# Performance work log

Measured on AMD Instinct MI355X. Metric: run time of the kernel, lower is better.

## Reference

```python
import jax, jax.numpy as jnp
import numpy as np

G_NUM = 32768      # graphs
NPG = 32           # nodes per graph
EPG = 128          # edges per graph
H = 128            # hidden
N = G_NUM * NPG
E = G_NUM * EPG


def setup_inputs() -> dict:
    key = jax.random.key(0)
    ks = jax.random.split(key, 8)
    x = jax.random.normal(ks[0], (N, H), dtype=jnp.float32)
    W1 = jax.random.normal(ks[1], (H, H), dtype=jnp.float32) * (1.0 / np.sqrt(H))
    b1 = jnp.zeros((H,), jnp.float32)
    W2 = jax.random.normal(ks[2], (H, 2), dtype=jnp.float32) * (1.0 / np.sqrt(H))
    b2 = jnp.zeros((2,), jnp.float32)
    # standard gumbel noise for F.gumbel_softmax(tau=1)
    u = jax.random.uniform(ks[3], (N, 2), dtype=jnp.float32, minval=1e-6, maxval=1.0 - 1e-6)
    gumbel_noise = -jnp.log(-jnp.log(u))
    uniform_noise = jax.random.uniform(ks[4], (N, H), dtype=jnp.float32)  # torch.rand_like
    # intra-graph random edges: graph g owns nodes [g*NPG, (g+1)*NPG)
    offs = jnp.repeat(jnp.arange(G_NUM, dtype=jnp.int32) * NPG, EPG)
    src = offs + jax.random.randint(ks[5], (E,), 0, NPG, dtype=jnp.int32)
    dst = offs + jax.random.randint(ks[6], (E,), 0, NPG, dtype=jnp.int32)
    edge_index = jnp.stack([src, dst])
    batch = jnp.repeat(jnp.arange(G_NUM, dtype=jnp.int32), NPG)
    return {"x": x, "W1": W1, "b1": b1, "W2": W2, "b2": b2,
            "gumbel_noise": gumbel_noise, "uniform_noise": uniform_noise,
            "edge_index": edge_index, "batch": batch, "num_graphs": G_NUM}


def reference(x, W1, b1, W2, b2, gumbel_noise, uniform_noise, edge_index, batch, num_graphs):
    eps = 1e-7
    G = int(num_graphs)
    Hd = x.shape[1]
    seg = lambda v: jax.ops.segment_sum(v, batch, num_segments=G)
    counts = seg(jnp.ones((x.shape[0],), x.dtype))                  # [G]
    # detached per-graph std/mean (torch.std_mean, unbiased)
    sx = jax.lax.stop_gradient(x)
    mean = seg(sx) / counts[:, None]                                # [G,H]
    var = seg((sx - mean[batch]) ** 2) / (counts - 1.0)[:, None]
    std = jnp.sqrt(var)                                             # [G,H]
    # soft assignment + gumbel-softmax (tau=1, logits = softmax probs, as in source)
    abstract1 = jnp.tanh(x @ W1 + b1)
    assignment = jax.nn.softmax(abstract1 @ W2 + b2, axis=1)        # [N,2]
    gum = jax.nn.softmax(assignment + gumbel_noise, axis=-1)        # [N,2]
    lam_pos = gum[:, :1]
    lam_neg = gum[:, 1:2]
    mean_n = mean[batch]
    std_n = std[batch]
    noisy_mean = lam_pos * x + lam_neg * mean_n                     # [N,H]
    noisy_std = lam_neg * std_n                                     # [N,H]
    noisy = noisy_mean + uniform_noise * noisy_std
    graph_emb = seg(x)                                              # [G,H]
    noisy_emb = seg(noisy)                                          # [G,H]
    # KL: 0.5*noisy_std^2/(std+eps)^2 (per node) + sum_nodes(((noisy_mean-mean)/(std+eps))^2) (per graph, broadcast)
    term1 = 0.5 * noisy_std ** 2 / (std_n + eps) ** 2               # [N,H]
    term2 = seg(((noisy_mean - mean_n) / (std_n + eps)) ** 2)       # [G,H]
    kl_g = (jnp.sum(seg(term1), axis=1) + counts * jnp.sum(term2, axis=1)) / (counts * Hd)
    kl_loss = jnp.mean(kl_g)
    # pooled adjacency: assignment^T A assignment per graph, via edge list
    src, dst = edge_index[0], edge_index[1]
    e_g = batch[src]
    contrib = assignment[src][:, :, None] * assignment[dst][:, None, :]  # [E,2,2]
    new_adj = jax.ops.segment_sum(contrib, e_g, num_segments=G)          # [G,2,2]
    row_l1 = jnp.maximum(jnp.sum(jnp.abs(new_adj), axis=2, keepdims=True), 1e-12)
    norm_adj = new_adj / row_l1
    diag = jnp.diagonal(norm_adj, axis1=1, axis2=2)                 # [G,2]
    pos_penalty = jnp.mean(jnp.mean((diag - 1.0) ** 2, axis=1))
    preserve_g = seg((assignment[:, 0] > 0.5).astype(x.dtype)) / counts
    preserve_rate = jnp.mean(preserve_g)
    active = lam_pos[:, 0] > 0.5                                    # [N] node mask
    return graph_emb, noisy_emb, active, pos_penalty, kl_loss, preserve_rate
```

## Files before the change

### kernel.cpp

```cpp
#include <hip/hip_runtime.h>

#define HN   128
#define NPG  32
#define GP4  4
#define NT   512
#define SX   132
#define TILE (NPG * SX)

typedef float f4 __attribute__((ext_vector_type(4)));
typedef float f2 __attribute__((ext_vector_type(2)));

__global__ __launch_bounds__(NT, 2) void gib_main(
    const float* __restrict__ x,  const float* __restrict__ W1,
    const float* __restrict__ b1, const float* __restrict__ W2,
    const float* __restrict__ b2, const float* __restrict__ gn,
    const float* __restrict__ un, const int* __restrict__ ei,
    float* __restrict__ out, float* __restrict__ ws,
    int G, long E, int epg, int spb)
{
  const int t    = threadIdx.x;
  const int p    = t >> 7;
  const int lo   = t & 127;
  const int ng   = lo & 7;
  const int cg   = lo >> 3;
  const int wv   = t >> 6;
  const int lid  = t & 63;
  const int half = lo >> 6;
  const int fp   = lo & 63;

  __shared__ __align__(16) float W1s[HN * HN];
  __shared__ __align__(16) float xs[GP4 * TILE];
  __shared__ float zred[GP4][2][8][4][2];
  __shared__ float pA[GP4][2][HN], pB[GP4][2][HN];
  __shared__ float s_mean[GP4][HN], s_std[GP4][HN], s_iv[GP4][HN];
  __shared__ float s_a0[GP4][NPG], s_a1[GP4][NPG], s_lp[GP4][NPG], s_ln[GP4][NPG];
  __shared__ float t2p[GP4][2], sr2p[GP4], adjp[GP4][2][4], s_scal[GP4][3];

  const long GL = (long)G * HN;
  const int  g0 = blockIdx.x * (GP4 * spb);

  const f4 b1a = *(const f4*)(b1 + 8 * cg);
  const f4 b1b = *(const f4*)(b1 + 8 * cg + 4);
  float w2l[16];
  #pragma unroll
  for (int u = 0; u < 4; ++u) {
    f4 v = *(const f4*)(W2 + 16 * cg + 4 * u);
    w2l[4*u+0] = v[0]; w2l[4*u+1] = v[1]; w2l[4*u+2] = v[2]; w2l[4*u+3] = v[3];
  }
  const float b20 = b2[0], b21 = b2[1];

  #pragma unroll
  for (int r = 0; r < 8; ++r) {
    int s = r * NT + t;
    int k = s >> 5, gm = s & 31;
    int slot = ((gm & 1) << 4) | (gm >> 1);
    *(f4*)&W1s[k * HN + slot * 4] = *(const f4*)(W1 + s * 4);
  }
  #pragma unroll
  for (int r = 0; r < 8; ++r) {
    int s = r * NT + t;
    int pp = s >> 10, q = s & 1023, n = q >> 5, pc = q & 31;
    *(f4*)&xs[pp * TILE + n * SX + pc * 4] =
        *(const f4*)(x + ((long)(g0 + pp) * NPG + n) * HN + pc * 4);
  }
  __syncthreads();

  for (int si = 0; si < spb; ++si) {
    const int  gs = g0 + si * GP4;
    const int  g  = gs + p;
    const long nb = (long)g * NPG;
    const bool more = (si + 1 < spb);

    f4 xr[8];
    if (more) {
      #pragma unroll
      for (int r = 0; r < 8; ++r) {
        int s = r * NT + t;
        int pp = s >> 10, q = s & 1023, n = q >> 5, pc = q & 31;
        xr[r] = *(const f4*)(x + ((long)(gs + GP4 + pp) * NPG + n) * HN + pc * 4);
      }
    }
    f2 gnr = {0.f, 0.f};
    if (wv < GP4 && lid < NPG)
      gnr = *(const f2*)(gn + ((long)(gs + wv) * NPG + lid) * 2);

    {
      const float* xb = &xs[p * TILE + half * 16 * SX + 2 * fp];
      float s10 = 0.f, s11 = 0.f, s20 = 0.f, s21 = 0.f;
      #pragma unroll
      for (int it = 0; it < 16; ++it) {
        f2 v = *(const f2*)(xb + it * SX);
        s10 += v[0]; s11 += v[1];
        s20 = fmaf(v[0], v[0], s20);
        s21 = fmaf(v[1], v[1], s21);
      }
      f2 w0 = {s10, s11}, w1v = {s20, s21};
      *(f2*)&pA[p][half][2 * fp] = w0;
      *(f2*)&pB[p][half][2 * fp] = w1v;
    }

    f4 aa[4], ab[4];
    #pragma unroll
    for (int i = 0; i < 4; ++i) { aa[i] = b1a; ab[i] = b1b; }
    {
      const float* xb = &xs[p * TILE + ng * SX];
      const float* wb = &W1s[cg * 4];
      #pragma unroll 8
      for (int pc = 0; pc < 32; ++pc) {
        f4 xv0 = *(const f4*)(xb + pc * 4);
        f4 xv1 = *(const f4*)(xb + 8  * SX + pc * 4);
        f4 xv2 = *(const f4*)(xb + 16 * SX + pc * 4);
        f4 xv3 = *(const f4*)(xb + 24 * SX + pc * 4);
        #pragma unroll
        for (int j = 0; j < 4; ++j) {
          f4 wa  = *(const f4*)(wb + (4 * pc + j) * HN);
          f4 wbv = *(const f4*)(wb + (4 * pc + j) * HN + 64);
          aa[0] += wa * xv0[j]; ab[0] += wbv * xv0[j];
          aa[1] += wa * xv1[j]; ab[1] += wbv * xv1[j];
          aa[2] += wa * xv2[j]; ab[2] += wbv * xv2[j];
          aa[3] += wa * xv3[j]; ab[3] += wbv * xv3[j];
        }
      }
    }
    #pragma unroll
    for (int i = 0; i < 4; ++i) {
      float z0 = 0.f, z1 = 0.f;
      #pragma unroll
      for (int u = 0; u < 4; ++u) {
        float h = tanhf(aa[i][u]);
        z0 = fmaf(h, w2l[2 * u], z0);
        z1 = fmaf(h, w2l[2 * u + 1], z1);
      }
      #pragma unroll
      for (int u = 0; u < 4; ++u) {
        float h = tanhf(ab[i][u]);
        z0 = fmaf(h, w2l[8 + 2 * u], z0);
        z1 = fmaf(h, w2l[9 + 2 * u], z1);
      }
      #pragma unroll
      for (int m = 8; m <= 32; m <<= 1) {
        z0 += __shfl_xor(z0, m, 64);
        z1 += __shfl_xor(z1, m, 64);
      }
      if (lid < 8) { zred[p][half][ng][i][0] = z0; zred[p][half][ng][i][1] = z1; }
    }
    __syncthreads();

    if (wv < GP4) {
      const int gq = gs + wv;
      f2 sa0 = *(const f2*)&pA[wv][0][2 * lid];
      f2 sa1 = *(const f2*)&pA[wv][1][2 * lid];
      f2 sb0 = *(const f2*)&pB[wv][0][2 * lid];
      f2 sb1 = *(const f2*)&pB[wv][1][2 * lid];
      float s10 = sa0[0] + sa1[0], s11 = sa0[1] + sa1[1];
      float s20 = sb0[0] + sb1[0], s21 = sb0[1] + sb1[1];
      float mean0 = s10 * (1.f / NPG), mean1 = s11 * (1.f / NPG);
      float var0 = fmaxf((s20 - s10 * mean0) * (1.f / (NPG - 1)), 0.f);
      float var1 = fmaxf((s21 - s11 * mean1) * (1.f / (NPG - 1)), 0.f);
      float sd0 = sqrtf(var0), sd1 = sqrtf(var1);
      float inv0 = 1.f / (sd0 + 1e-7f), inv1 = 1.f / (sd1 + 1e-7f);
      f2 mv = {mean0, mean1}, sv = {sd0, sd1}, iv = {inv0 * inv0, inv1 * inv1};
      *(f2*)&s_mean[wv][2 * lid] = mv;
      *(f2*)&s_std [wv][2 * lid] = sv;
      *(f2*)&s_iv  [wv][2 * lid] = iv;
      f2 ge = {s10, s11};
      *(f2*)&out[(long)gq * HN + 2 * lid] = ge;
      float r0 = sd0 * inv0, r1 = sd1 * inv1;
      float r2 = r0 * r0 + r1 * r1;
      #pragma unroll
      for (int m = 1; m <= 32; m <<= 1) r2 += __shfl_xor(r2, m, 64);
      if (lid == 0) sr2p[wv] = r2;
      if (lid < NPG) {
        const int n = lid;
        float z0 = b20 + zred[wv][0][n & 7][n >> 3][0] + zred[wv][1][n & 7][n >> 3][0];
        float z1 = b21 + zred[wv][0][n & 7][n >> 3][1] + zred[wv][1][n & 7][n >> 3][1];
        float zm = fmaxf(z0, z1);
        float e0 = expf(z0 - zm), e1 = expf(z1 - zm);
        float a0 = e0 / (e0 + e1), a1 = 1.f - a0;
        float q0 = a0 + gnr[0], q1 = a1 + gnr[1];
        float qm = fmaxf(q0, q1);
        float E0 = expf(q0 - qm), E1 = expf(q1 - qm);
        float lp = E0 / (E0 + E1), ln = 1.f - lp;
        s_a0[wv][n] = a0; s_a1[wv][n] = a1; s_lp[wv][n] = lp; s_ln[wv][n] = ln;
        out[2 * GL + (long)gq * NPG + n] = (lp > 0.5f) ? 1.0f : 0.0f;
        float v1 = ln, v2 = ln * ln, v3 = (a0 > 0.5f) ? 1.f : 0.f;
        #pragma unroll
        for (int m = 1; m <= 16; m <<= 1) {
          v1 += __shfl_xor(v1, m, 64);
          v2 += __shfl_xor(v2, m, 64);
          v3 += __shfl_xor(v3, m, 64);
        }
        if (n == 0) { s_scal[wv][0] = v1; s_scal[wv][1] = v2; s_scal[wv][2] = v3; }
      }
    }
    __syncthreads();

    {
      f2 ur[16];
      #pragma unroll
      for (int it = 0; it < 16; ++it)
        ur[it] = *(const f2*)(un + (nb + half * 16 + it) * HN + 2 * fp);
      int es = 0, ed = 0;
      if (lo < epg) {
        es = ei[(long)g * epg + lo] - g * NPG;
        ed = ei[E + (long)g * epg + lo] - g * NPG;
      }
      const float* xb = &xs[p * TILE + half * 16 * SX + 2 * fp];
      f2 mu = *(const f2*)&s_mean[p][2 * fp];
      f2 iv = *(const f2*)&s_iv[p][2 * fp];
      float tv = 0.f, A0 = 0.f, A1 = 0.f, B0 = 0.f, B1 = 0.f;
      #pragma unroll
      for (int it = 0; it < 16; ++it) {
        const int n = half * 16 + it;
        f2 v = *(const f2*)(xb + it * SX);
        float lpn = s_lp[p][n], lnn = s_ln[p][n];
        float d0 = v[0] - mu[0], d1 = v[1] - mu[1];
        tv = fmaf(lpn * lpn, fmaf(d0 * d0, iv[0], d1 * d1 * iv[1]), tv);
        A0 = fmaf(lpn, v[0], A0); A1 = fmaf(lpn, v[1], A1);
        B0 = fmaf(lnn, ur[it][0], B0); B1 = fmaf(lnn, ur[it][1], B1);
      }
      #pragma unroll
      for (int m = 1; m <= 32; m <<= 1) tv += __shfl_xor(tv, m, 64);
      if (lid == 0) t2p[p][half] = tv;
      f2 wA = {A0, A1}, wB = {B0, B1};
      *(f2*)&pA[p][half][2 * fp] = wA;
      *(f2*)&pB[p][half][2 * fp] = wB;
      float c00 = 0.f, c01 = 0.f, c10 = 0.f, c11 = 0.f;
      if (lo < epg) {
        float as0 = s_a0[p][es], as1 = s_a1[p][es];
        float ad0 = s_a0[p][ed], ad1 = s_a1[p][ed];
        c00 = as0 * ad0; c01 = as0 * ad1; c10 = as1 * ad0; c11 = as1 * ad1;
      }
      for (int e = 128 + lo; e < epg; e += 128) {
        int s2 = ei[(long)g * epg + e] - g * NPG;
        int d2 = ei[E + (long)g * epg + e] - g * NPG;
        float as0 = s_a0[p][s2], as1 = s_a1[p][s2];
        float ad0 = s_a0[p][d2], ad1 = s_a1[p][d2];
        c00 = fmaf(as0, ad0, c00); c01 = fmaf(as0, ad1, c01);
        c10 = fmaf(as1, ad0, c10); c11 = fmaf(as1, ad1, c11);
      }
      #pragma unroll
      for (int m = 1; m <= 32; m <<= 1) {
        c00 += __shfl_xor(c00, m, 64); c01 += __shfl_xor(c01, m, 64);
        c10 += __shfl_xor(c10, m, 64); c11 += __shfl_xor(c11, m, 64);
      }
      if (lid == 0) {
        adjp[p][half][0] = c00; adjp[p][half][1] = c01;
        adjp[p][half][2] = c10; adjp[p][half][3] = c11;
      }
    }
    __syncthreads();

    if (wv < GP4) {
      const int gq = gs + wv;
      f2 a0v = *(const f2*)&pA[wv][0][2 * lid];
      f2 a1v = *(const f2*)&pA[wv][1][2 * lid];
      f2 b0v = *(const f2*)&pB[wv][0][2 * lid];
      f2 b1v2 = *(const f2*)&pB[wv][1][2 * lid];
      f2 mu = *(const f2*)&s_mean[wv][2 * lid];
      f2 sd = *(const f2*)&s_std[wv][2 * lid];
      float SLN = s_scal[wv][0];
      f2 ne;
      ne[0] = fmaf(mu[0], SLN, a0v[0] + a1v[0]) + sd[0] * (b0v[0] + b1v2[0]);
      ne[1] = fmaf(mu[1], SLN, a0v[1] + a1v[1]) + sd[1] * (b0v[1] + b1v2[1]);
      *(f2*)&out[GL + (long)gq * HN + 2 * lid] = ne;
      if (lid == 32) {
        float a00 = adjp[wv][0][0] + adjp[wv][1][0];
        float a01 = adjp[wv][0][1] + adjp[wv][1][1];
        float a10 = adjp[wv][0][2] + adjp[wv][1][2];
        float a11 = adjp[wv][0][3] + adjp[wv][1][3];
        float d0 = a00 / fmaxf(fabsf(a00) + fabsf(a01), 1e-12f);
        float d1 = a11 / fmaxf(fabsf(a10) + fabsf(a11), 1e-12f);
        float pen = 0.5f * ((d0 - 1.f) * (d0 - 1.f) + (d1 - 1.f) * (d1 - 1.f));
        float t2 = t2p[wv][0] + t2p[wv][1];
        float kl = (0.5f * s_scal[wv][1] * sr2p[wv] + (float)NPG * t2) / (float)(NPG * HN);
        ws[gq]                 = kl;
        ws[(size_t)G + gq]     = pen;
        ws[2 * (size_t)G + gq] = s_scal[wv][2] * (1.0f / NPG);
      }
    }
    if (more) {
      #pragma unroll
      for (int r = 0; r < 8; ++r) {
        int s = r * NT + t;
        int pp = s >> 10, q = s & 1023, n = q >> 5, pc = q & 31;
        *(f4*)&xs[pp * TILE + n * SX + pc * 4] = xr[r];
      }
    }
    __syncthreads();
  }
}

__global__ __launch_bounds__(1024) void gib_final(const float* __restrict__ ws,
                                                  float* __restrict__ out,
                                                  int G, long base)
{
  __shared__ float red[3][16];
  const int t = threadIdx.x, w = t >> 6, lid = t & 63;
  float s0 = 0.f, s1 = 0.f, s2 = 0.f;
  for (int i = t; i < G; i += 1024) {
    s0 += ws[(size_t)G + i];
    s1 += ws[i];
    s2 += ws[2 * (size_t)G + i];
  }
  #pragma unroll
  for (int m = 1; m <= 32; m <<= 1) {
    s0 += __shfl_xor(s0, m, 64);
    s1 += __shfl_xor(s1, m, 64);
    s2 += __shfl_xor(s2, m, 64);
  }
  if (lid == 0) { red[0][w] = s0; red[1][w] = s1; red[2][w] = s2; }
  __syncthreads();
  if (t == 0) {
    float r0 = 0.f, r1 = 0.f, r2 = 0.f;
    for (int i = 0; i < 16; ++i) { r0 += red[0][i]; r1 += red[1][i]; r2 += red[2][i]; }
    out[base + 0] = r0 / (float)G;
    out[base + 1] = r1 / (float)G;
    out[base + 2] = r2 / (float)G;
  }
}

extern "C" void kernel_launch(void* const* d_in, const int* in_sizes, int n_in,
                              void* d_out, int out_size, void* d_ws, size_t ws_size,
                              hipStream_t stream)
{
  const float* x  = (const float*)d_in[0];
  const float* W1 = (const float*)d_in[1];
  const float* b1 = (const float*)d_in[2];
  const float* W2 = (const float*)d_in[3];
  const float* b2 = (const float*)d_in[4];
  const float* gn = (const float*)d_in[5];
  const float* un = (const float*)d_in[6];
  const int*   ei = (const int*)d_in[7];
  float* out = (float*)d_out;
  float* ws  = (float*)d_ws;

  const long N = (long)in_sizes[0] / HN;
  const int  G = (int)(N / NPG);
  const long E = (long)in_sizes[7] / 2;
  const int epg = (int)(E / G);

  const int spb = 8;
  const int nblocks = G / (GP4 * spb);
  hipLaunchKernelGGL(gib_main, dim3(nblocks), dim3(NT), 0, stream,
                     x, W1, b1, W2, b2, gn, un, ei, out, ws, G, E, epg, spb);
  const long base = 2L * (long)G * HN + N;
  hipLaunchKernelGGL(gib_final, dim3(1), dim3(1024), 0, stream, ws, out, G, base);
}
```

Baseline: 750.8 us.

## Assign one graph per wavefront with half-width x tiles, removing block barriers

Restructures the main kernel so each 64-lane wavefront processes its own stream of 16 graphs instead of four graphs sharing a 512-thread block. Every per-graph reduction now uses wave shuffles, so all __syncthreads inside the loop are gone. The x tile is staged in shared memory in two 64-column halves that are reloaded from global during the computation, which shrinks LDS per wave. The cost is that x is read from global twice per graph (the next graph's first half is prefetched), register pressure is higher with 8x8 accumulators per lane, and the launch-bounds occupancy hint is dropped.

```diff
diff --git a/kernel.cpp b/kernel.cpp
--- a/kernel.cpp
+++ b/kernel.cpp
@@ -1,53 +1,38 @@
 #include <hip/hip_runtime.h>
 
-#define HN   128
-#define NPG  32
-#define GP4  4
-#define NT   512
-#define SX   132
-#define TILE (NPG * SX)
+#define HN  128
+#define NPG 32
+#define HK  64
+#define SXH 68
+#define NT  512
+#define NW  8
+#define SPG 16
 
 typedef float f4 __attribute__((ext_vector_type(4)));
 typedef float f2 __attribute__((ext_vector_type(2)));
 
-__global__ __launch_bounds__(NT, 2) void gib_main(
+__global__ __launch_bounds__(NT) void gib_main(
     const float* __restrict__ x,  const float* __restrict__ W1,
     const float* __restrict__ b1, const float* __restrict__ W2,
     const float* __restrict__ b2, const float* __restrict__ gn,
     const float* __restrict__ un, const int* __restrict__ ei,
     float* __restrict__ out, float* __restrict__ ws,
-    int G, long E, int epg, int spb)
+    int G, long E, int epg)
 {
-  const int t    = threadIdx.x;
-  const int p    = t >> 7;
-  const int lo   = t & 127;
-  const int ng   = lo & 7;
-  const int cg   = lo >> 3;
-  const int wv   = t >> 6;
-  const int lid  = t & 63;
-  const int half = lo >> 6;
-  const int fp   = lo & 63;
+  const int t  = threadIdx.x;
+  const int wv = t >> 6;
+  const int l  = t & 63;
+  const int ng = l & 3;
+  const int cg = l >> 2;
+  const int cp = l & 31;
+  const int nh = l >> 5;
 
   __shared__ __align__(16) float W1s[HN * HN];
-  __shared__ __align__(16) float xs[GP4 * TILE];
-  __shared__ float zred[GP4][2][8][4][2];
-  __shared__ float pA[GP4][2][HN], pB[GP4][2][HN];
-  __shared__ float s_mean[GP4][HN], s_std[GP4][HN], s_iv[GP4][HN];
-  __shared__ float s_a0[GP4][NPG], s_a1[GP4][NPG], s_lp[GP4][NPG], s_ln[GP4][NPG];
-  __shared__ float t2p[GP4][2], sr2p[GP4], adjp[GP4][2][4], s_scal[GP4][3];
+  __shared__ __align__(16) float xs[NW][NPG * SXH];
+  __shared__ float s_mean[NW][HN], s_std[NW][HN], s_iv[NW][HN];
+  __shared__ float s_lp[NW][NPG], s_a0[NW][NPG];
 
   const long GL = (long)G * HN;
-  const int  g0 = blockIdx.x * (GP4 * spb);
-
-  const f4 b1a = *(const f4*)(b1 + 8 * cg);
-  const f4 b1b = *(const f4*)(b1 + 8 * cg + 4);
-  float w2l[16];
-  #pragma unroll
-  for (int u = 0; u < 4; ++u) {
-    f4 v = *(const f4*)(W2 + 16 * cg + 4 * u);
-    w2l[4*u+0] = v[0]; w2l[4*u+1] = v[1]; w2l[4*u+2] = v[2]; w2l[4*u+3] = v[3];
-  }
-  const float b20 = b2[0], b21 = b2[1];
 
   #pragma unroll
   for (int r = 0; r < 8; ++r) {
@@ -56,186 +41,240 @@
     int slot = ((gm & 1) << 4) | (gm >> 1);
     *(f4*)&W1s[k * HN + slot * 4] = *(const f4*)(W1 + s * 4);
   }
+  __syncthreads();
+
+  float* xh = &xs[wv][0];
+
+  const f4 b1A = *(const f4*)(b1 + 8 * cg);
+  const f4 b1B = *(const f4*)(b1 + 8 * cg + 4);
+  f4 w2q[4];
   #pragma unroll
-  for (int r = 0; r < 8; ++r) {
-    int s = r * NT + t;
-    int pp = s >> 10, q = s & 1023, n = q >> 5, pc = q & 31;
-    *(f4*)&xs[pp * TILE + n * SX + pc * 4] =
-        *(const f4*)(x + ((long)(g0 + pp) * NPG + n) * HN + pc * 4);
-  }
-  __syncthreads();
-
-  for (int si = 0; si < spb; ++si) {
-    const int  gs = g0 + si * GP4;
-    const int  g  = gs + p;
-    const long nb = (long)g * NPG;
-    const bool more = (si + 1 < spb);
-
-    f4 xr[8];
-    if (more) {
-      #pragma unroll
-      for (int r = 0; r < 8; ++r) {
-        int s = r * NT + t;
-        int pp = s >> 10, q = s & 1023, n = q >> 5, pc = q & 31;
-        xr[r] = *(const f4*)(x + ((long)(gs + GP4 + pp) * NPG + n) * HN + pc * 4);
-      }
-    }
-    f2 gnr = {0.f, 0.f};
-    if (wv < GP4 && lid < NPG)
-      gnr = *(const f2*)(gn + ((long)(gs + wv) * NPG + lid) * 2);
-
+  for (int u = 0; u < 4; ++u) w2q[u] = *(const f4*)(W2 + 16 * cg + 4 * u);
+  const float b20 = b2[0], b21 = b2[1];
+
+  const long gbase = ((long)blockIdx.x * NW + wv) * SPG;
+  const int sr = l >> 4, sc = l & 15;
+
+  {
+    const float* xg = x + gbase * NPG * HN;
+    #pragma unroll
+    for (int r = 0; r < 8; ++r) {
+      int n = r + 8 * sr;
+      f4 v = *(const f4*)(xg + n * HN + sc * 4);
+      *(f4*)&xh[n * SXH + sc * 4] = v;
+    }
+  }
+
+  for (int si = 0; si < SPG; ++si) {
+    const long g = gbase + si;
+    if (g >= G) break;
+    const long nb = g * NPG;
+    const float* xg = x + nb * HN;
+
+    f4 Lh[8];
+    #pragma unroll
+    for (int r = 0; r < 8; ++r)
+      Lh[r] = *(const f4*)(xg + (r + 8 * sr) * HN + HK + sc * 4);
+    f2 gnr[8];
+    if (l < 4) {
+      #pragma unroll
+      for (int i = 0; i < 8; ++i)
+        gnr[i] = *(const f2*)(gn + (nb + l + 4 * i) * 2);
+    }
+
+    f2 s1h0 = {0.f, 0.f}, sqh0 = {0.f, 0.f};
+    #pragma unroll
+    for (int i = 0; i < 16; ++i) {
+      f2 v = *(const f2*)&xh[(nh * 16 + i) * SXH + 2 * cp];
+      s1h0[0] += v[0]; s1h0[1] += v[1];
+      sqh0[0] = fmaf(v[0], v[0], sqh0[0]);
+      sqh0[1] = fmaf(v[1], v[1], sqh0[1]);
+    }
+
+    f4 accA[8], accB[8];
+    #pragma unroll
+    for (int i = 0; i < 8; ++i) { accA[i] = b1A; accB[i] = b1B; }
+    #pragma unroll 4
+    for (int kc = 0; kc < 16; ++kc) {
+      const int kr = kc * 4;
+      f4 wA0 = *(const f4*)&W1s[(kr + 0) * HN + cg * 4];
+      f4 wA1 = *(const f4*)&W1s[(kr + 1) * HN + cg * 4];
+      f4 wA2 = *(const f4*)&W1s[(kr + 2) * HN + cg * 4];
+      f4 wA3 = *(const f4*)&W1s[(kr + 3) * HN + cg * 4];
+      f4 wB0 = *(const f4*)&W1s[(kr + 0) * HN + 64 + cg * 4];
+      f4 wB1 = *(const f4*)&W1s[(kr + 1) * HN + 64 + cg * 4];
+      f4 wB2 = *(const f4*)&W1s[(kr + 2) * HN + 64 + cg * 4];
+      f4 wB3 = *(const f4*)&W1s[(kr + 3) * HN + 64 + cg * 4];
+      #pragma unroll
+      for (int i = 0; i < 8; ++i) {
+        f4 xv = *(const f4*)&xh[(ng + 4 * i) * SXH + kc * 4];
+        accA[i] += wA0 * xv[0]; accB[i] += wB0 * xv[0];
+        accA[i] += wA1 * xv[1]; accB[i] += wB1 * xv[1];
+        accA[i] += wA2 * xv[2]; accB[i] += wB2 * xv[2];
+        accA[i] += wA3 * xv[3]; accB[i] += wB3 * xv[3];
+      }
+    }
+
+    #pragma unroll
+    for (int r = 0; r < 8; ++r)
+      *(f4*)&xh[(r + 8 * sr) * SXH + sc * 4] = Lh[r];
+    f4 Lh2[8];
+    #pragma unroll
+    for (int r = 0; r < 8; ++r)
+      Lh2[r] = *(const f4*)(xg + (r + 8 * sr) * HN + sc * 4);
+    int es0 = 0, ed0 = 0, es1 = 0, ed1 = 0;
+    if (l < epg)      { es0 = ei[g * epg + l];      ed0 = ei[E + g * epg + l]; }
+    if (l + 64 < epg) { es1 = ei[g * epg + l + 64]; ed1 = ei[E + g * epg + l + 64]; }
+
+    f2 s1h1 = {0.f, 0.f}, sqh1 = {0.f, 0.f};
+    #pragma unroll
+    for (int i = 0; i < 16; ++i) {
+      f2 v = *(const f2*)&xh[(nh * 16 + i) * SXH + 2 * cp];
+      s1h1[0] += v[0]; s1h1[1] += v[1];
+      sqh1[0] = fmaf(v[0], v[0], sqh1[0]);
+      sqh1[1] = fmaf(v[1], v[1], sqh1[1]);
+    }
+
+    #pragma unroll 4
+    for (int kc = 0; kc < 16; ++kc) {
+      const int kr = (HK + kc * 4);
+      f4 wA0 = *(const f4*)&W1s[(kr + 0) * HN + cg * 4];
+      f4 wA1 = *(const f4*)&W1s[(kr + 1) * HN + cg * 4];
+      f4 wA2 = *(const f4*)&W1s[(kr + 2) * HN + cg * 4];
+      f4 wA3 = *(const f4*)&W1s[(kr + 3) * HN + cg * 4];
+      f4 wB0 = *(const f4*)&W1s[(kr + 0) * HN + 64 + cg * 4];
+      f4 wB1 = *(const f4*)&W1s[(kr + 1) * HN + 64 + cg * 4];
+      f4 wB2 = *(const f4*)&W1s[(kr + 2) * HN + 64 + cg * 4];
+      f4 wB3 = *(const f4*)&W1s[(kr + 3) * HN + 64 + cg * 4];
+      #pragma unroll
+      for (int i = 0; i < 8; ++i) {
+        f4 xv = *(const f4*)&xh[(ng + 4 * i) * SXH + kc * 4];
+        accA[i] += wA0 * xv[0]; accB[i] += wB0 * xv[0];
+        accA[i] += wA1 * xv[1]; accB[i] += wB1 * xv[1];
+        accA[i] += wA2 * xv[2]; accB[i] += wB2 * xv[2];
+        accA[i] += wA3 * xv[3]; accB[i] += wB3 * xv[3];
+      }
+    }
+
+    float r2acc = 0.f;
     {
-      const float* xb = &xs[p * TILE + half * 16 * SX + 2 * fp];
-      float s10 = 0.f, s11 = 0.f, s20 = 0.f, s21 = 0.f;
-      #pragma unroll
-      for (int it = 0; it < 16; ++it) {
-        f2 v = *(const f2*)(xb + it * SX);
-        s10 += v[0]; s11 += v[1];
-        s20 = fmaf(v[0], v[0], s20);
-        s21 = fmaf(v[1], v[1], s21);
-      }
-      f2 w0 = {s10, s11}, w1v = {s20, s21};
-      *(f2*)&pA[p][half][2 * fp] = w0;
-      *(f2*)&pB[p][half][2 * fp] = w1v;
-    }
-
-    f4 aa[4], ab[4];
-    #pragma unroll
-    for (int i = 0; i < 4; ++i) { aa[i] = b1a; ab[i] = b1b; }
-    {
-      const float* xb = &xs[p * TILE + ng * SX];
-      const float* wb = &W1s[cg * 4];
-      #pragma unroll 8
-      for (int pc = 0; pc < 32; ++pc) {
-        f4 xv0 = *(const f4*)(xb + pc * 4);
-        f4 xv1 = *(const f4*)(xb + 8  * SX + pc * 4);
-        f4 xv2 = *(const f4*)(xb + 16 * SX + pc * 4);
-        f4 xv3 = *(const f4*)(xb + 24 * SX + pc * 4);
-        #pragma unroll
-        for (int j = 0; j < 4; ++j) {
-          f4 wa  = *(const f4*)(wb + (4 * pc + j) * HN);
-          f4 wbv = *(const f4*)(wb + (4 * pc + j) * HN + 64);
-          aa[0] += wa * xv0[j]; ab[0] += wbv * xv0[j];
-          aa[1] += wa * xv1[j]; ab[1] += wbv * xv1[j];
-          aa[2] += wa * xv2[j]; ab[2] += wbv * xv2[j];
-          aa[3] += wa * xv3[j]; ab[3] += wbv * xv3[j];
+      #pragma unroll
+      for (int h = 0; h < 2; ++h) {
+        f2 s1 = h ? s1h1 : s1h0, sq = h ? sqh1 : sqh0;
+        float a0s = s1[0] + __shfl_xor(s1[0], 32, 64);
+        float a1s = s1[1] + __shfl_xor(s1[1], 32, 64);
+        float q0s = sq[0] + __shfl_xor(sq[0], 32, 64);
+        float q1s = sq[1] + __shfl_xor(sq[1], 32, 64);
+        float m0 = a0s * (1.f / NPG), m1 = a1s * (1.f / NPG);
+        float v0 = fmaxf((q0s - a0s * m0) * (1.f / (NPG - 1)), 0.f);
+        float v1 = fmaxf((q1s - a1s * m1) * (1.f / (NPG - 1)), 0.f);
+        float sd0 = sqrtf(v0), sd1 = sqrtf(v1);
+        float in0 = 1.f / (sd0 + 1e-7f), in1 = 1.f / (sd1 + 1e-7f);
+        if (l < 32) {
+          f2 mv = {m0, m1}, sv = {sd0, sd1}, iv = {in0 * in0, in1 * in1};
+          *(f2*)&s_mean[wv][h * HK + 2 * cp] = mv;
+          *(f2*)&s_std [wv][h * HK + 2 * cp] = sv;
+          *(f2*)&s_iv  [wv][h * HK + 2 * cp] = iv;
+          f2 ge = {a0s, a1s};
+          *(f2*)&out[g * HN + h * HK + 2 * cp] = ge;
         }
-      }
-    }
-    #pragma unroll
-    for (int i = 0; i < 4; ++i) {
-      float z0 = 0.f, z1 = 0.f;
-      #pragma unroll
-      for (int u = 0; u < 4; ++u) {
-        float h = tanhf(aa[i][u]);
-        z0 = fmaf(h, w2l[2 * u], z0);
-        z1 = fmaf(h, w2l[2 * u + 1], z1);
-      }
-      #pragma unroll
-      for (int u = 0; u < 4; ++u) {
-        float h = tanhf(ab[i][u]);
-        z0 = fmaf(h, w2l[8 + 2 * u], z0);
-        z1 = fmaf(h, w2l[9 + 2 * u], z1);
-      }
-      #pragma unroll
-      for (int m = 8; m <= 32; m <<= 1) {
+        float r0 = sd0 * in0, r1 = sd1 * in1;
+        r2acc += r0 * r0 + r1 * r1;
+      }
+      #pragma unroll
+      for (int m = 1; m <= 16; m <<= 1) r2acc += __shfl_xor(r2acc, m, 64);
+    }
+
+    float zz0[8], zz1[8];
+    #pragma unroll
+    for (int i = 0; i < 8; ++i) {
+      float h0 = tanhf(accA[i][0]), h1 = tanhf(accA[i][1]);
+      float h2 = tanhf(accA[i][2]), h3 = tanhf(accA[i][3]);
+      float h4 = tanhf(accB[i][0]), h5 = tanhf(accB[i][1]);
+      float h6 = tanhf(accB[i][2]), h7 = tanhf(accB[i][3]);
+      float z0 = h0 * w2q[0][0] + h1 * w2q[0][2] + h2 * w2q[1][0] + h3 * w2q[1][2]
+               + h4 * w2q[2][0] + h5 * w2q[2][2] + h6 * w2q[3][0] + h7 * w2q[3][2];
+      float z1 = h0 * w2q[0][1] + h1 * w2q[0][3] + h2 * w2q[1][1] + h3 * w2q[1][3]
+               + h4 * w2q[2][1] + h5 * w2q[2][3] + h6 * w2q[3][1] + h7 * w2q[3][3];
+      #pragma unroll
+      for (int m = 4; m <= 32; m <<= 1) {
         z0 += __shfl_xor(z0, m, 64);
         z1 += __shfl_xor(z1, m, 64);
       }
-      if (lid < 8) { zred[p][half][ng][i][0] = z0; zred[p][half][ng][i][1] = z1; }
-    }
-    __syncthreads();
-
-    if (wv < GP4) {
-      const int gq = gs + wv;
-      f2 sa0 = *(const f2*)&pA[wv][0][2 * lid];
-      f2 sa1 = *(const f2*)&pA[wv][1][2 * lid];
-      f2 sb0 = *(const f2*)&pB[wv][0][2 * lid];
-      f2 sb1 = *(const f2*)&pB[wv][1][2 * lid];
-      float s10 = sa0[0] + sa1[0], s11 = sa0[1] + sa1[1];
-      float s20 = sb0[0] + sb1[0], s21 = sb0[1] + sb1[1];
-      float mean0 = s10 * (1.f / NPG), mean1 = s11 * (1.f / NPG);
-      float var0 = fmaxf((s20 - s10 * mean0) * (1.f / (NPG - 1)), 0.f);
-      float var1 = fmaxf((s21 - s11 * mean1) * (1.f / (NPG - 1)), 0.f);
-      float sd0 = sqrtf(var0), sd1 = sqrtf(var1);
-      float inv0 = 1.f / (sd0 + 1e-7f), inv1 = 1.f / (sd1 + 1e-7f);
-      f2 mv = {mean0, mean1}, sv = {sd0, sd1}, iv = {inv0 * inv0, inv1 * inv1};
-      *(f2*)&s_mean[wv][2 * lid] = mv;
-      *(f2*)&s_std [wv][2 * lid] = sv;
-      *(f2*)&s_iv  [wv][2 * lid] = iv;
-      f2 ge = {s10, s11};
-      *(f2*)&out[(long)gq * HN + 2 * lid] = ge;
-      float r0 = sd0 * inv0, r1 = sd1 * inv1;
-      float r2 = r0 * r0 + r1 * r1;
-      #pragma unroll
-      for (int m = 1; m <= 32; m <<= 1) r2 += __shfl_xor(r2, m, 64);
-      if (lid == 0) sr2p[wv] = r2;
-      if (lid < NPG) {
-        const int n = lid;
-        float z0 = b20 + zred[wv][0][n & 7][n >> 3][0] + zred[wv][1][n & 7][n >> 3][0];
-        float z1 = b21 + zred[wv][0][n & 7][n >> 3][1] + zred[wv][1][n & 7][n >> 3][1];
+      zz0[i] = z0; zz1[i] = z1;
+    }
+
+    float vSLN = 0.f, vSLN2 = 0.f, vpres = 0.f;
+    if (l < 4) {
+      #pragma unroll
+      for (int i = 0; i < 8; ++i) {
+        const int n = l + 4 * i;
+        float z0 = b20 + zz0[i], z1 = b21 + zz1[i];
         float zm = fmaxf(z0, z1);
         float e0 = expf(z0 - zm), e1 = expf(z1 - zm);
         float a0 = e0 / (e0 + e1), a1 = 1.f - a0;
-        float q0 = a0 + gnr[0], q1 = a1 + gnr[1];
+        float q0 = a0 + gnr[i][0], q1 = a1 + gnr[i][1];
         float qm = fmaxf(q0, q1);
         float E0 = expf(q0 - qm), E1 = expf(q1 - qm);
         float lp = E0 / (E0 + E1), ln = 1.f - lp;
-        s_a0[wv][n] = a0; s_a1[wv][n] = a1; s_lp[wv][n] = lp; s_ln[wv][n] = ln;
-        out[2 * GL + (long)gq * NPG + n] = (lp > 0.5f) ? 1.0f : 0.0f;
-        float v1 = ln, v2 = ln * ln, v3 = (a0 > 0.5f) ? 1.f : 0.f;
-        #pragma unroll
-        for (int m = 1; m <= 16; m <<= 1) {
-          v1 += __shfl_xor(v1, m, 64);
-          v2 += __shfl_xor(v2, m, 64);
-          v3 += __shfl_xor(v3, m, 64);
-        }
-        if (n == 0) { s_scal[wv][0] = v1; s_scal[wv][1] = v2; s_scal[wv][2] = v3; }
-      }
-    }
-    __syncthreads();
-
+        s_lp[wv][n] = lp; s_a0[wv][n] = a0;
+        out[2 * GL + nb + n] = (lp > 0.5f) ? 1.0f : 0.0f;
+        vSLN += ln; vSLN2 += ln * ln; vpres += (a0 > 0.5f) ? 1.f : 0.f;
+      }
+      vSLN  += __shfl_xor(vSLN, 1, 64);  vSLN  += __shfl_xor(vSLN, 2, 64);
+      vSLN2 += __shfl_xor(vSLN2, 1, 64); vSLN2 += __shfl_xor(vSLN2, 2, 64);
+      vpres += __shfl_xor(vpres, 1, 64); vpres += __shfl_xor(vpres, 2, 64);
+    }
+    const float SLN = __shfl(vSLN, 0, 64);
+
+    float tv = 0.f;
     {
       f2 ur[16];
       #pragma unroll
-      for (int it = 0; it < 16; ++it)
-        ur[it] = *(const f2*)(un + (nb + half * 16 + it) * HN + 2 * fp);
-      int es = 0, ed = 0;
-      if (lo < epg) {
-        es = ei[(long)g * epg + lo] - g * NPG;
-        ed = ei[E + (long)g * epg + lo] - g * NPG;
-      }
-      const float* xb = &xs[p * TILE + half * 16 * SX + 2 * fp];
-      f2 mu = *(const f2*)&s_mean[p][2 * fp];
-      f2 iv = *(const f2*)&s_iv[p][2 * fp];
-      float tv = 0.f, A0 = 0.f, A1 = 0.f, B0 = 0.f, B1 = 0.f;
-      #pragma unroll
-      for (int it = 0; it < 16; ++it) {
-        const int n = half * 16 + it;
-        f2 v = *(const f2*)(xb + it * SX);
-        float lpn = s_lp[p][n], lnn = s_ln[p][n];
+      for (int i = 0; i < 16; ++i)
+        ur[i] = *(const f2*)(un + (nb + nh * 16 + i) * HN + HK + 2 * cp);
+      f2 mu = *(const f2*)&s_mean[wv][HK + 2 * cp];
+      f2 iv = *(const f2*)&s_iv [wv][HK + 2 * cp];
+      float A0 = 0.f, A1 = 0.f, B0 = 0.f, B1 = 0.f;
+      #pragma unroll
+      for (int i = 0; i < 16; ++i) {
+        const int n = nh * 16 + i;
+        f2 v = *(const f2*)&xh[n * SXH + 2 * cp];
+        float lpn = s_lp[wv][n], lnn = 1.f - lpn;
         float d0 = v[0] - mu[0], d1 = v[1] - mu[1];
         tv = fmaf(lpn * lpn, fmaf(d0 * d0, iv[0], d1 * d1 * iv[1]), tv);
         A0 = fmaf(lpn, v[0], A0); A1 = fmaf(lpn, v[1], A1);
-        B0 = fmaf(lnn, ur[it][0], B0); B1 = fmaf(lnn, ur[it][1], B1);
-      }
-      #pragma unroll
-      for (int m = 1; m <= 32; m <<= 1) tv += __shfl_xor(tv, m, 64);
-      if (lid == 0) t2p[p][half] = tv;
-      f2 wA = {A0, A1}, wB = {B0, B1};
-      *(f2*)&pA[p][half][2 * fp] = wA;
-      *(f2*)&pB[p][half][2 * fp] = wB;
-      float c00 = 0.f, c01 = 0.f, c10 = 0.f, c11 = 0.f;
-      if (lo < epg) {
-        float as0 = s_a0[p][es], as1 = s_a1[p][es];
-        float ad0 = s_a0[p][ed], ad1 = s_a1[p][ed];
+        B0 = fmaf(lnn, ur[i][0], B0); B1 = fmaf(lnn, ur[i][1], B1);
+      }
+      A0 += __shfl_xor(A0, 32, 64); A1 += __shfl_xor(A1, 32, 64);
+      B0 += __shfl_xor(B0, 32, 64); B1 += __shfl_xor(B1, 32, 64);
+      if (l < 32) {
+        f2 sd = *(const f2*)&s_std[wv][HK + 2 * cp];
+        f2 ne = {fmaf(mu[0], SLN, A0) + sd[0] * B0,
+                 fmaf(mu[1], SLN, A1) + sd[1] * B1};
+        *(f2*)&out[GL + g * HN + HK + 2 * cp] = ne;
+      }
+    }
+
+    float c00 = 0.f, c01 = 0.f, c10 = 0.f, c11 = 0.f;
+    {
+      if (l < epg) {
+        int s2 = es0 - (int)nb, d2 = ed0 - (int)nb;
+        float as0 = s_a0[wv][s2], as1 = 1.f - as0;
+        float ad0 = s_a0[wv][d2], ad1 = 1.f - ad0;
         c00 = as0 * ad0; c01 = as0 * ad1; c10 = as1 * ad0; c11 = as1 * ad1;
       }
-      for (int e = 128 + lo; e < epg; e += 128) {
-        int s2 = ei[(long)g * epg + e] - g * NPG;
-        int d2 = ei[E + (long)g * epg + e] - g * NPG;
-        float as0 = s_a0[p][s2], as1 = s_a1[p][s2];
-        float ad0 = s_a0[p][d2], ad1 = s_a1[p][d2];
+      if (l + 64 < epg) {
+        int s2 = es1 - (int)nb, d2 = ed1 - (int)nb;
+        float as0 = s_a0[wv][s2], as1 = 1.f - as0;
+        float ad0 = s_a0[wv][d2], ad1 = 1.f - ad0;
+        c00 = fmaf(as0, ad0, c00); c01 = fmaf(as0, ad1, c01);
+        c10 = fmaf(as1, ad0, c10); c11 = fmaf(as1, ad1, c11);
+      }
+      for (int e = 128 + l; e < epg; e += 64) {
+        int s2 = ei[g * epg + e] - (int)nb, d2 = ei[E + g * epg + e] - (int)nb;
+        float as0 = s_a0[wv][s2], as1 = 1.f - as0;
+        float ad0 = s_a0[wv][d2], ad1 = 1.f - ad0;
         c00 = fmaf(as0, ad0, c00); c01 = fmaf(as0, ad1, c01);
         c10 = fmaf(as1, ad0, c10); c11 = fmaf(as1, ad1, c11);
       }
@@ -244,50 +283,60 @@
         c00 += __shfl_xor(c00, m, 64); c01 += __shfl_xor(c01, m, 64);
         c10 += __shfl_xor(c10, m, 64); c11 += __shfl_xor(c11, m, 64);
       }
-      if (lid == 0) {
-        adjp[p][half][0] = c00; adjp[p][half][1] = c01;
-        adjp[p][half][2] = c10; adjp[p][half][3] = c11;
-      }
-    }
-    __syncthreads();
-
-    if (wv < GP4) {
-      const int gq = gs + wv;
-      f2 a0v = *(const f2*)&pA[wv][0][2 * lid];
-      f2 a1v = *(const f2*)&pA[wv][1][2 * lid];
-      f2 b0v = *(const f2*)&pB[wv][0][2 * lid];
-      f2 b1v2 = *(const f2*)&pB[wv][1][2 * lid];
-      f2 mu = *(const f2*)&s_mean[wv][2 * lid];
-      f2 sd = *(const f2*)&s_std[wv][2 * lid];
-      float SLN = s_scal[wv][0];
-      f2 ne;
-      ne[0] = fmaf(mu[0], SLN, a0v[0] + a1v[0]) + sd[0] * (b0v[0] + b1v2[0]);
-      ne[1] = fmaf(mu[1], SLN, a0v[1] + a1v[1]) + sd[1] * (b0v[1] + b1v2[1]);
-      *(f2*)&out[GL + (long)gq * HN + 2 * lid] = ne;
-      if (lid == 32) {
-        float a00 = adjp[wv][0][0] + adjp[wv][1][0];
-        float a01 = adjp[wv][0][1] + adjp[wv][1][1];
-        float a10 = adjp[wv][0][2] + adjp[wv][1][2];
-        float a11 = adjp[wv][0][3] + adjp[wv][1][3];
-        float d0 = a00 / fmaxf(fabsf(a00) + fabsf(a01), 1e-12f);
-        float d1 = a11 / fmaxf(fabsf(a10) + fabsf(a11), 1e-12f);
-        float pen = 0.5f * ((d0 - 1.f) * (d0 - 1.f) + (d1 - 1.f) * (d1 - 1.f));
-        float t2 = t2p[wv][0] + t2p[wv][1];
-        float kl = (0.5f * s_scal[wv][1] * sr2p[wv] + (float)NPG * t2) / (float)(NPG * HN);
-        ws[gq]                 = kl;
-        ws[(size_t)G + gq]     = pen;
-        ws[2 * (size_t)G + gq] = s_scal[wv][2] * (1.0f / NPG);
-      }
-    }
-    if (more) {
-      #pragma unroll
-      for (int r = 0; r < 8; ++r) {
-        int s = r * NT + t;
-        int pp = s >> 10, q = s & 1023, n = q >> 5, pc = q & 31;
-        *(f4*)&xs[pp * TILE + n * SX + pc * 4] = xr[r];
-      }
-    }
-    __syncthreads();
+    }
+
+    #pragma unroll
+    for (int r = 0; r < 8; ++r)
+      *(f4*)&xh[(r + 8 * sr) * SXH + sc * 4] = Lh2[r];
+    const long gnx = (g + 1 < G) ? (g + 1) : g;
+    f4 Lh3[8];
+    #pragma unroll
+    for (int r = 0; r < 8; ++r)
+      Lh3[r] = *(const f4*)(x + (gnx * NPG + r + 8 * sr) * HN + sc * 4);
+
+    {
+      f2 ur[16];
+      #pragma unroll
+      for (int i = 0; i < 16; ++i)
+        ur[i] = *(const f2*)(un + (nb + nh * 16 + i) * HN + 2 * cp);
+      f2 mu = *(const f2*)&s_mean[wv][2 * cp];
+      f2 iv = *(const f2*)&s_iv [wv][2 * cp];
+      float A0 = 0.f, A1 = 0.f, B0 = 0.f, B1 = 0.f;
+      #pragma unroll
+      for (int i = 0; i < 16; ++i) {
+        const int n = nh * 16 + i;
+        f2 v = *(const f2*)&xh[n * SXH + 2 * cp];
+        float lpn = s_lp[wv][n], lnn = 1.f - lpn;
+        float d0 = v[0] - mu[0], d1 = v[1] - mu[1];
+        tv = fmaf(lpn * lpn, fmaf(d0 * d0, iv[0], d1 * d1 * iv[1]), tv);
+        A0 = fmaf(lpn, v[0], A0); A1 = fmaf(lpn, v[1], A1);
+        B0 = fmaf(lnn, ur[i][0], B0); B1 = fmaf(lnn, ur[i][1], B1);
+      }
+      A0 += __shfl_xor(A0, 32, 64); A1 += __shfl_xor(A1, 32, 64);
+      B0 += __shfl_xor(B0, 32, 64); B1 += __shfl_xor(B1, 32, 64);
+      if (l < 32) {
+        f2 sd = *(const f2*)&s_std[wv][2 * cp];
+        f2 ne = {fmaf(mu[0], SLN, A0) + sd[0] * B0,
+                 fmaf(mu[1], SLN, A1) + sd[1] * B1};
+        *(f2*)&out[GL + g * HN + 2 * cp] = ne;
+      }
+    }
+    #pragma unroll
+    for (int m = 1; m <= 32; m <<= 1) tv += __shfl_xor(tv, m, 64);
+
+    if (l == 0) {
+      float d0 = c00 / fmaxf(fabsf(c00) + fabsf(c01), 1e-12f);
+      float d1 = c11 / fmaxf(fabsf(c10) + fabsf(c11), 1e-12f);
+      float pen = 0.5f * ((d0 - 1.f) * (d0 - 1.f) + (d1 - 1.f) * (d1 - 1.f));
+      float kl = (0.5f * vSLN2 * r2acc + (float)NPG * tv) / (float)(NPG * HN);
+      ws[g]                 = kl;
+      ws[(size_t)G + g]     = pen;
+      ws[2 * (size_t)G + g] = vpres * (1.0f / NPG);
+    }
+
+    #pragma unroll
+    for (int r = 0; r < 8; ++r)
+      *(f4*)&xh[(r + 8 * sr) * SXH + sc * 4] = Lh3[r];
   }
 }
 
@@ -340,10 +389,9 @@
   const long E = (long)in_sizes[7] / 2;
   const int epg = (int)(E / G);
 
-  const int spb = 8;
-  const int nblocks = G / (GP4 * spb);
+  const int nblocks = (G + NW * SPG - 1) / (NW * SPG);
   hipLaunchKernelGGL(gib_main, dim3(nblocks), dim3(NT), 0, stream,
-                     x, W1, b1, W2, b2, gn, un, ei, out, ws, G, E, epg, spb);
+                     x, W1, b1, W2, b2, gn, un, ei, out, ws, G, E, epg);
   const long base = 2L * (long)G * HN + N;
   hipLaunchKernelGGL(gib_final, dim3(1), dim3(1024), 0, stream, ws, out, G, base);
 }
```

Measured after the change: 901.1 us. +20.0%, slower.
